# Kernel tuning notes

Hardware: AMD Instinct MI355X
Metric: run time of the kernel (lower is better)

## Reference

```python
import jax, jax.numpy as jnp
from jax import lax
import numpy as np

IN_SIZE, H_SIZE, OUT_SIZE, SEAS = 48, 128, 48, 24
DILATIONS = (1, 2, 4, 8)  # cells 0-1 = DRNN group 0, cells 2-3 = DRNN group 1


def setup_inputs() -> dict:
    key = jax.random.key(0)
    ks = jax.random.split(key, 16)
    B, T = 256, 512
    inp = {
        'train': jax.random.uniform(ks[0], (B, T), jnp.float32, 0.5, 1.5),
        'val': jax.random.uniform(ks[1], (B, OUT_SIZE), jnp.float32, 0.5, 1.5),
        'test': jax.random.uniform(ks[2], (B, OUT_SIZE), jnp.float32, 0.5, 1.5),
        'init_lev_sm': jnp.array([0.5], jnp.float32),
        'init_seas_sm': jnp.array([0.5], jnp.float32),
        'init_seasonalities': jnp.full((SEAS,), 0.5, jnp.float32),
    }
    cin = [IN_SIZE, H_SIZE, H_SIZE, H_SIZE]
    k = 3
    for i in range(4):
        inp[f'w_ih{i}'] = jax.random.normal(ks[k], (4 * H_SIZE, cin[i]), jnp.float32) * 0.05; k += 1
        inp[f'w_hh{i}'] = jax.random.normal(ks[k], (4 * H_SIZE, H_SIZE), jnp.float32) * 0.05; k += 1
        inp[f'b_ih{i}'] = jnp.zeros((4 * H_SIZE,), jnp.float32)
        inp[f'b_hh{i}'] = jnp.zeros((4 * H_SIZE,), jnp.float32)
    inp['nl_w'] = jax.random.normal(ks[k], (H_SIZE, H_SIZE), jnp.float32) * 0.05; k += 1
    inp['nl_b'] = jnp.zeros((H_SIZE,), jnp.float32)
    inp['sc_w'] = jax.random.normal(ks[k], (OUT_SIZE, H_SIZE), jnp.float32) * 0.05; k += 1
    inp['sc_b'] = jnp.zeros((OUT_SIZE,), jnp.float32)
    return inp


def _lstm(x, w_ih, w_hh, b_ih, b_hh):
    # x: (T, N, C) -> (T, N, H); torch LSTM gate order i, f, g, o
    n, h = x.shape[1], w_hh.shape[1]

    def step(carry, xt):
        hp, cp = carry
        g = xt @ w_ih.T + hp @ w_hh.T + (b_ih + b_hh)
        i, f, gg, o = jnp.split(g, 4, axis=-1)
        c = jax.nn.sigmoid(f) * cp + jax.nn.sigmoid(i) * jnp.tanh(gg)
        hn = jax.nn.sigmoid(o) * jnp.tanh(c)
        return (hn, c), hn

    z = jnp.zeros((n, h), x.dtype)
    _, hs = lax.scan(step, (z, z), x)
    return hs


def _dilated_lstm(x, d, w_ih, w_hh, b_ih, b_hh):
    # DRNN dilation: fold time by d into batch, run cell, unfold
    t, b, c = x.shape
    td = -(-t // d) * d
    xp = jnp.pad(x, ((0, td - t), (0, 0), (0, 0)))
    xd = xp.reshape(td // d, d, b, c).reshape(td // d, d * b, c)
    out = _lstm(xd, w_ih, w_hh, b_ih, b_hh)
    h = out.shape[-1]
    return out.reshape(td // d, d, b, h).reshape(td, b, h)[:t]


def _series_forward(data, cells, nl_w, nl_b, sc_w, sc_b):
    # ResidualDRNN: group 0 (cells 0,1), group 1 (cells 2,3) with residual add
    x = data
    for grp in range(2):
        res = x
        for ci in (2 * grp, 2 * grp + 1):
            x = _dilated_lstm(x, DILATIONS[ci], *cells[ci])
        if grp > 0:
            x = x + res
    x = jnp.tanh(x @ nl_w.T + nl_b)
    return x @ sc_w.T + sc_b


def _esrnn(train, val, init_lev_sm, init_seas_sm, init_seasonalities, cells, nl_w, nl_b, sc_w, sc_b):
    B, T = train.shape
    lev_sm = jax.nn.sigmoid(init_lev_sm[0])
    seas_sm = jax.nn.sigmoid(init_seas_sm[0])
    s0 = jnp.exp(init_seasonalities)  # (SEAS,) shared across series
    lev0 = train[:, 0] / s0[0]  # (B,)
    # rolling buffer: at step i it holds seasonalities[i .. i+SEAS-1]
    buf0 = jnp.broadcast_to(jnp.concatenate([s0[1:], s0[:1]])[:, None], (SEAS, B))

    def step(carry, x_t):
        lev_p, buf = carry
        seas_t = buf[0]
        lev_n = lev_sm * (x_t / seas_t) + (1 - lev_sm) * lev_p
        seas_n = seas_sm * (x_t / lev_n) + (1 - seas_sm) * seas_t
        return (lev_n, jnp.concatenate([buf[1:], seas_n[None]], 0)), (lev_n, seas_n)

    _, (levs_r, seas_r) = lax.scan(step, (lev0, buf0), train[:, 1:].T)
    levs = jnp.concatenate([lev0[None], levs_r], 0).T  # (B, T)
    seas_head = jnp.broadcast_to(jnp.concatenate([s0, s0[:1]])[:, None], (SEAS + 1, B))
    seas = jnp.concatenate([seas_head, seas_r], 0).T  # (B, T+SEAS)
    if OUT_SIZE > SEAS:  # seasonality extension branch
        start = seas.shape[1] - SEAS
        seas = jnp.concatenate([seas, seas[:, start:start + OUT_SIZE - SEAS]], 1)
    W = T - IN_SIZE + 1
    Wo = T - OUT_SIZE - IN_SIZE + 1
    idx_in = jnp.arange(W)[:, None] + jnp.arange(IN_SIZE)[None, :]  # (W, IN)
    win_in = (train[:, idx_in] / seas[:, idx_in] / levs[:, IN_SIZE - 1:, None]).transpose(1, 0, 2)  # (W,B,IN)
    idx_out = jnp.arange(Wo)[:, None] + IN_SIZE + jnp.arange(OUT_SIZE)[None, :]
    win_out = (train[:, idx_out] / seas[:, idx_out] / levs[:, IN_SIZE - 1:IN_SIZE - 1 + Wo, None]).transpose(1, 0, 2)
    network_pred = _series_forward(win_in[:-OUT_SIZE], cells, nl_w, nl_b, sc_w, sc_b)  # (Wo,B,OUT)
    network_act = win_out
    net_out_all = _series_forward(win_in, cells, nl_w, nl_b, sc_w, sc_b)  # (W,B,OUT)
    hold = net_out_all[-1] * seas[:, -OUT_SIZE:] * levs[:, -1:]
    hold_out_pred = hold * (hold > 0).astype(hold.dtype)
    hold_out_act = val  # testing=False path
    hold_out_act_norm = val / seas[:, -OUT_SIZE:] / levs[:, -1:]
    return network_pred, network_act, hold_out_pred, net_out_all, hold_out_act, hold_out_act_norm


def reference(train, val, test, init_lev_sm, init_seas_sm, init_seasonalities,
              w_ih0, w_hh0, b_ih0, b_hh0, w_ih1, w_hh1, b_ih1, b_hh1,
              w_ih2, w_hh2, b_ih2, b_hh2, w_ih3, w_hh3, b_ih3, b_hh3,
              nl_w, nl_b, sc_w, sc_b):
    cells = ((w_ih0, w_hh0, b_ih0, b_hh0), (w_ih1, w_hh1, b_ih1, b_hh1),
             (w_ih2, w_hh2, b_ih2, b_hh2), (w_ih3, w_hh3, b_ih3, b_hh3))
    return _esrnn(train, val, init_lev_sm, init_seas_sm, init_seasonalities,
                  cells, nl_w, nl_b, sc_w, sc_b)
```

## Files before the change

kernel.cpp:

```cpp
#include <hip/hip_runtime.h>
#include <cstdint>
#include <cstddef>

typedef _Float16 half8 __attribute__((ext_vector_type(8)));
typedef _Float16 half4 __attribute__((ext_vector_type(4)));
typedef float floatx4 __attribute__((ext_vector_type(4)));

namespace {
constexpr int kB = 256, kT = 512, kIN = 48, kOUT = 48, kSEAS = 24, kH = 128;
constexpr int kW = kT - kIN + 1;
constexpr int kWO = kT - kOUT - kIN + 1;
constexpr int kNB = kW * kB;
constexpr int kMBLK = kNB / 16;
constexpr float kLOG2E = 1.44269504088896340736f;
}

#if __has_builtin(__builtin_amdgcn_exp2f)
#define FEXP2(x) __builtin_amdgcn_exp2f(x)
#else
#define FEXP2(x) exp2f(x)
#endif
#if __has_builtin(__builtin_amdgcn_rcpf)
#define FRCP(x) __builtin_amdgcn_rcpf(x)
#else
#define FRCP(x) (1.0f / (x))
#endif

__device__ __forceinline__ float fsig(float y) { return FRCP(1.0f + FEXP2(-y)); }
__device__ __forceinline__ float ftanh(float x) { return 2.0f * fsig(2.0f * kLOG2E * x) - 1.0f; }

__global__ void k_transpose(const float* __restrict__ train, float* __restrict__ trainT) {
  int t = blockIdx.x, b = threadIdx.x;
  trainT[t * kB + b] = train[b * kT + t];
}

__global__ void k_es(const float* __restrict__ trainT, const float* __restrict__ levp,
                     const float* __restrict__ seasp, const float* __restrict__ inits,
                     float* __restrict__ seas, float* __restrict__ levs) {
  __shared__ float ring[kSEAS][kB];
  int b = threadIdx.x;
  float lev_sm = fsig(levp[0] * kLOG2E);
  float seas_sm = fsig(seasp[0] * kLOG2E);
  float s00 = expf(inits[0]);
  for (int s = 0; s < kSEAS; ++s) {
    float v = expf(inits[s]);
    seas[s * kB + b] = v;
    if (s >= 1) ring[s - 1][b] = v;
  }
  ring[kSEAS - 1][b] = s00;
  seas[kSEAS * kB + b] = s00;
  float lev = trainT[b] * FRCP(s00);
  levs[b] = lev;
  int rk = 0;
  float x_nx = trainT[kB + b];
  float st_nx = ring[0][b];
  for (int k = 0; k < kT - 1; ++k) {
    float x = x_nx;
    float st = st_nx;
    if (k + 1 < kT - 1) x_nx = trainT[(k + 2) * kB + b];
    int rn = (rk + 1 == kSEAS) ? 0 : rk + 1;
    st_nx = ring[rn][b];
    float ln = lev_sm * (x * FRCP(st)) + (1.0f - lev_sm) * lev;
    float sn = seas_sm * (x * FRCP(ln)) + (1.0f - seas_sm) * st;
    ring[rk][b] = sn;
    seas[(k + kSEAS + 1) * kB + b] = sn;
    levs[(k + 1) * kB + b] = ln;
    lev = ln;
    rk = rn;
  }
  for (int j = 0; j < kOUT - kSEAS; ++j)
    seas[(kT + kSEAS + j) * kB + b] = seas[(kT + j) * kB + b];
}

__global__ void k_win_in(const float* __restrict__ trainT, const float* __restrict__ seas,
                         const float* __restrict__ levs, _Float16* __restrict__ win) {
  int w = blockIdx.x;
  int tid = threadIdx.x;
#pragma unroll
  for (int i = 0; i < 16; ++i) {
    int o = i * 256 + tid;
    int b = o >> 3;
    int j0 = (o & 7) * 8;
    half8 h;
    if (j0 < kIN) {
      float rl = FRCP(levs[(kIN - 1 + w) * kB + b]);
#pragma unroll
      for (int jj = 0; jj < 8; ++jj) {
        int j = j0 + jj;
        int t = w + j;
        float v = (j < kIN) ? trainT[t * kB + b] * FRCP(seas[t * kB + b]) * rl : 0.0f;
        h[jj] = (_Float16)v;
      }
    } else {
#pragma unroll
      for (int jj = 0; jj < 8; ++jj) h[jj] = (_Float16)0.0f;
    }
    *(half8*)(win + ((size_t)(w * kB + b)) * 64 + j0) = h;
  }
}

__global__ void k_win_out(const float* __restrict__ trainT, const float* __restrict__ seas,
                          const float* __restrict__ levs, float* __restrict__ out1) {
  int idx = blockIdx.x * 256 + threadIdx.x;
  if (idx >= kWO * kB * (kOUT / 4)) return;
  int row = idx / 12;
  int j0 = (idx - row * 12) * 4;
  int wo = row >> 8;
  int b = row & 255;
  float rl = FRCP(levs[(kIN - 1 + wo) * kB + b]);
  floatx4 v;
#pragma unroll
  for (int jj = 0; jj < 4; ++jj) {
    int t = kIN + wo + j0 + jj;
    v[jj] = trainT[t * kB + b] * FRCP(seas[t * kB + b]) * rl;
  }
  *(floatx4*)(out1 + (size_t)row * kOUT + j0) = v;
}

__device__ __forceinline__ void prep_bias_elem(const float* bih, const float* bhh, float* dst,
                                               int c) {
  int ct = c >> 4, n16 = c & 15, g = ct & 3, wv = ct >> 2;
  int row = g * 128 + wv * 16 + n16;
  float sc = (g == 2) ? 2.0f * kLOG2E : kLOG2E;
  dst[c] = (bih[row] + bhh[row]) * sc;
}

__device__ __forceinline__ void prep_frag_elem(const float* Wsrc, _Float16* dst, int KB, int Kreal,
                                               int srcld, int perm, int idx) {
  int jj = idx & 7;
  int lane = (idx >> 3) & 63;
  int kb = (idx >> 9) % KB;
  int ct = idx / (KB * 512);
  int n16 = lane & 15;
  int k = kb * 32 + ((lane >> 4) << 3) + jj;
  int row;
  float sc;
  if (perm) {
    int g = ct & 3, wv = ct >> 2;
    row = g * 128 + wv * 16 + n16;
    sc = (g == 2) ? 2.0f * kLOG2E : kLOG2E;
  } else {
    row = ct * 16 + n16;
    sc = 1.0f;
  }
  float v = (k < Kreal) ? Wsrc[row * srcld + k] * sc : 0.0f;
  dst[idx] = (_Float16)v;
}

struct PrepArgs {
  const float* bih[4];
  const float* bhh[4];
  float* biasp[4];
  const float* wih[4];
  _Float16* wihf[4];
  const float* whh[4];
  _Float16* whhf[4];
  const float* nlw;
  _Float16* nlf;
  const float* scw;
  _Float16* scf;
};

__global__ void k_prep_all(PrepArgs a) {
  int seg = blockIdx.y;
  int idx = blockIdx.x * 256 + threadIdx.x;
  if (seg < 4) {
    if (idx < 512) prep_bias_elem(a.bih[seg], a.bhh[seg], a.biasp[seg], idx);
  } else if (seg == 4) {
    if (idx < 32 * 2 * 512) prep_frag_elem(a.wih[0], a.wihf[0], 2, 48, 48, 1, idx);
  } else if (seg < 8) {
    int c = seg - 4;
    if (idx < 32 * 4 * 512) prep_frag_elem(a.wih[c], a.wihf[c], 4, 128, 128, 1, idx);
  } else if (seg < 12) {
    int c = seg - 8;
    if (idx < 32 * 4 * 512) prep_frag_elem(a.whh[c], a.whhf[c], 4, 128, 128, 1, idx);
  } else if (seg == 12) {
    if (idx < 8 * 4 * 512) prep_frag_elem(a.nlw, a.nlf, 4, 128, 128, 0, idx);
  } else {
    if (idx < 3 * 4 * 512) prep_frag_elem(a.scw, a.scf, 4, 128, 128, 0, idx);
  }
}

__global__ void k_zero_prog(int* prog) {
  int i = threadIdx.x;
  if (i < 192) prog[i] = 0;
}

template <int NT, int KB, int MODE>
__global__ __launch_bounds__(512) void k_gemm(const _Float16* __restrict__ A,
                                              const _Float16* __restrict__ A2, int Khalfs,
                                              const _Float16* __restrict__ Bfr,
                                              const float* __restrict__ bias,
                                              _Float16* __restrict__ outh,
                                              float* __restrict__ outf,
                                              float* __restrict__ outf2) {
  __shared__ _Float16 bsh[NT * KB * 512];
  int tid = threadIdx.x;
  {
    const uint4* src = (const uint4*)Bfr;
    uint4* dst = (uint4*)bsh;
    for (int i = tid; i < NT * KB * 64; i += 512) dst[i] = src[i];
  }
  __syncthreads();
  int wv = tid >> 6, lane = tid & 63;
  int mblk = blockIdx.x * 8 + wv;
  if (mblk >= kMBLK) return;
  int m = lane & 15, kq = lane >> 4;
  const _Float16* arow = A + (size_t)(mblk * 16 + m) * Khalfs + kq * 8;
  half8 af[KB];
#pragma unroll
  for (int kb = 0; kb < KB; ++kb) af[kb] = *(const half8*)(arow + kb * 32);
  if constexpr (MODE == 1) {
    const _Float16* arow2 = A2 + (size_t)(mblk * 16 + m) * Khalfs + kq * 8;
#pragma unroll
    for (int kb = 0; kb < KB; ++kb) {
      half8 a2 = *(const half8*)(arow2 + kb * 32);
      af[kb] += a2;
    }
  }
#pragma unroll
  for (int t0 = 0; t0 < NT; t0 += 2) {
    float b0 = bias[t0 * 16 + m];
    floatx4 acc0 = {b0, b0, b0, b0};
    floatx4 acc1 = {0.f, 0.f, 0.f, 0.f};
    if (t0 + 1 < NT) {
      float b1 = bias[(t0 + 1) * 16 + m];
      acc1 = (floatx4){b1, b1, b1, b1};
    }
#pragma unroll
    for (int kb = 0; kb < KB; ++kb) {
      half8 bf0 = *(const half8*)(&bsh[((t0 * KB + kb) * 64 + lane) * 8]);
      acc0 = __builtin_amdgcn_mfma_f32_16x16x32_f16(af[kb], bf0, acc0, 0, 0, 0);
      if (t0 + 1 < NT) {
        half8 bf1 = *(const half8*)(&bsh[(((t0 + 1) * KB + kb) * 64 + lane) * 8]);
        acc1 = __builtin_amdgcn_mfma_f32_16x16x32_f16(af[kb], bf1, acc1, 0, 0, 0);
      }
    }
    if constexpr (MODE == 1) {
#pragma unroll
      for (int r = 0; r < 4; ++r) {
        int row = mblk * 16 + kq * 4 + r;
        outh[(size_t)row * kH + t0 * 16 + m] = (_Float16)ftanh(acc0[r]);
        if (t0 + 1 < NT) outh[(size_t)row * kH + (t0 + 1) * 16 + m] = (_Float16)ftanh(acc1[r]);
      }
    } else {
#pragma unroll
      for (int r = 0; r < 4; ++r) {
        int row = mblk * 16 + kq * 4 + r;
        float v0 = acc0[r];
        outf[(size_t)row * kOUT + t0 * 16 + m] = v0;
        if (row < kWO * kB) outf2[(size_t)row * kOUT + t0 * 16 + m] = v0;
        if (t0 + 1 < NT) {
          float v1 = acc1[r];
          outf[(size_t)row * kOUT + (t0 + 1) * 16 + m] = v1;
          if (row < kWO * kB) outf2[(size_t)row * kOUT + (t0 + 1) * 16 + m] = v1;
        }
      }
    }
  }
}

struct FArgs {
  const _Float16* win;
  const _Float16* wihf[4];
  const _Float16* whhf[4];
  const float* biasp[4];
  _Float16* H[4];
  int* prog;
};

__device__ __forceinline__ void wait_prog(int* p, int need, int& fenced, int* obs_sh) {
  if (need <= fenced) return;
  if (threadIdx.x == 0) {
    int v;
    while ((v = __hip_atomic_load(p, __ATOMIC_RELAXED, __HIP_MEMORY_SCOPE_AGENT)) < need)
      __builtin_amdgcn_s_sleep(16);
    *obs_sh = v;
  }
  __syncthreads();
  int v = *obs_sh;
  __builtin_amdgcn_fence(__ATOMIC_ACQUIRE, "agent");
  fenced = v;
}

template <int KXB, bool POLL, bool REL>
__device__ __forceinline__ void floop(const _Float16* __restrict__ Xsrc,
                                      const _Float16* __restrict__ wihp,
                                      const _Float16* __restrict__ whhp,
                                      const float* __restrict__ bp, _Float16* __restrict__ Hout,
                                      int* progIn, int sprev, int* progOut, int d, int kd, int ib,
                                      _Float16 (*hbuf)[2048], int* obs_sh) {
  int tid = threadIdx.x;
  int wv = tid >> 6, lane = tid & 63, m = lane & 15, kq = lane >> 4;
  half8 wxf[4][KXB], whf[4][4];
#pragma unroll
  for (int g = 0; g < 4; ++g) {
#pragma unroll
    for (int kb = 0; kb < KXB; ++kb)
      wxf[g][kb] = *(const half8*)(wihp + ((((wv * 4 + g) * KXB + kb) * 64 + lane) * 8));
#pragma unroll
    for (int kb = 0; kb < 4; ++kb)
      whf[g][kb] = *(const half8*)(whhp + ((((wv * 4 + g) * 4 + kb) * 64 + lane) * 8));
  }
  float bg[4];
#pragma unroll
  for (int g = 0; g < 4; ++g) bg[g] = bp[(wv * 4 + g) * 16 + m];
  float cc[4] = {0.f, 0.f, 0.f, 0.f};
  int nsteps = (kW - kd + d - 1) / d;
  const int xstride = KXB * 32;
  int fenced = 0;
  if (POLL) wait_prog(progIn + (kd & ((1 << sprev) - 1)), (kd >> sprev) + 1, fenced, obs_sh);
  half8 hxc[KXB], hxn[KXB];
  {
    const _Float16* xr = Xsrc + (size_t)(kd * kB + ib * 16 + m) * xstride + kq * 8;
#pragma unroll
    for (int kb = 0; kb < KXB; ++kb) hxc[kb] = *(const half8*)(xr + kb * 32);
  }
  for (int j = 0; j < nsteps; ++j) {
    int ph = j & 1;
    int wtn = (j + 1) * d + kd;
    bool havenext = (j + 1 < nsteps);
    if (POLL && havenext)
      wait_prog(progIn + (wtn & ((1 << sprev) - 1)), (wtn >> sprev) + 1, fenced, obs_sh);
    floatx4 acc[4];
#pragma unroll
    for (int g = 0; g < 4; ++g) acc[g] = (floatx4){bg[g], bg[g], bg[g], bg[g]};
    if (havenext) {
      const _Float16* xr = Xsrc + (size_t)(wtn * kB + ib * 16 + m) * xstride + kq * 8;
#pragma unroll
      for (int kb = 0; kb < KXB; ++kb) hxn[kb] = *(const half8*)(xr + kb * 32);
    }
#pragma unroll
    for (int kb = 0; kb < KXB; ++kb)
#pragma unroll
      for (int g = 0; g < 4; ++g)
        acc[g] = __builtin_amdgcn_mfma_f32_16x16x32_f16(hxc[kb], wxf[g][kb], acc[g], 0, 0, 0);
    if (j > 0) {
#pragma unroll
      for (int kb = 0; kb < 4; ++kb) {
        int gran = (kb * 4 + kq) ^ m;
        half8 a = *(const half8*)(&hbuf[ph ^ 1][m * 128 + gran * 8]);
#pragma unroll
        for (int g = 0; g < 4; ++g)
          acc[g] = __builtin_amdgcn_mfma_f32_16x16x32_f16(a, whf[g][kb], acc[g], 0, 0, 0);
      }
    }
#pragma unroll
    for (int r = 0; r < 4; ++r) {
      float iv = fsig(acc[0][r]);
      float fv = fsig(acc[1][r]);
      float g2 = fsig(acc[2][r]);
      float ov = fsig(acc[3][r]);
      cc[r] = fv * cc[r] + iv * (2.0f * g2 - 1.0f);
      float tc = 2.0f * fsig(cc[r] * (2.0f * kLOG2E)) - 1.0f;
      float hv = ov * tc;
      int brow = kq * 4 + r;
      int hu = wv * 16 + m;
      int gran = (hu >> 3) ^ brow;
      hbuf[ph][brow * 128 + gran * 8 + (hu & 7)] = (_Float16)hv;
    }
    __syncthreads();
    {
      int hr = tid >> 5, hu0 = (tid & 31) * 4;
      int gran = (hu0 >> 3) ^ hr;
      half4 hv4 = *(const half4*)(&hbuf[ph][hr * 128 + gran * 8 + (hu0 & 7)]);
      *(half4*)(Hout + (size_t)((j * d + kd) * kB + ib * 16 + hr) * kH + hu0) = hv4;
    }
    if (REL && (((j & 7) == 7) || (j + 1 == nsteps))) {
      __syncthreads();
      if (tid == 0)
        __hip_atomic_store(progOut, j + 1, __ATOMIC_RELEASE, __HIP_MEMORY_SCOPE_AGENT);
    }
#pragma unroll
    for (int kb = 0; kb < KXB; ++kb) hxc[kb] = hxn[kb];
  }
}

__global__ __launch_bounds__(512) void k_fused(FArgs a) {
  __shared__ _Float16 hbuf[2][2048];
  __shared__ int obs_sh;
  int w = blockIdx.x;
  int cell, d, kd, ib;
  if (w < 16) {
    cell = 0; d = 1; kd = 0; ib = w;
  } else if (w < 48) {
    cell = 1; d = 2; kd = (w - 16) >> 4; ib = (w - 16) & 15;
  } else if (w < 112) {
    cell = 2; d = 4; kd = (w - 48) >> 4; ib = (w - 48) & 15;
  } else {
    cell = 3; d = 8; kd = (w - 112) >> 4; ib = (w - 112) & 15;
  }
  const _Float16* Xsrc = (cell == 0) ? a.win : a.H[cell - 1];
  _Float16* Hout = a.H[cell];
  int* progOut = a.prog + (cell * 16 + ib) * 4 + kd;
  int* progIn = (cell > 0) ? a.prog + ((cell - 1) * 16 + ib) * 4 : nullptr;
  int sprev = (cell == 2) ? 1 : ((cell == 3) ? 2 : 0);
  if (cell == 0)
    floop<2, false, true>(Xsrc, a.wihf[0], a.whhf[0], a.biasp[0], Hout, nullptr, 0, progOut, d,
                          kd, ib, hbuf, &obs_sh);
  else if (cell < 3)
    floop<4, true, true>(Xsrc, a.wihf[cell], a.whhf[cell], a.biasp[cell], Hout, progIn, sprev,
                         progOut, d, kd, ib, hbuf, &obs_sh);
  else
    floop<4, true, false>(Xsrc, a.wihf[3], a.whhf[3], a.biasp[3], Hout, progIn, sprev, progOut,
                          d, kd, ib, hbuf, &obs_sh);
}

__global__ void k_tail(const float* __restrict__ out3, const float* __restrict__ val,
                       const float* __restrict__ seas, const float* __restrict__ levs,
                       float* __restrict__ out2, float* __restrict__ out4,
                       float* __restrict__ out5) {
  int idx = blockIdx.x * 256 + threadIdx.x;
  int b = idx / kOUT, j = idx % kOUT;
  float s = seas[(kT + j) * kB + b];
  float L = levs[(kT - 1) * kB + b];
  float net = out3[(size_t)(kW - 1) * kB * kOUT + idx];
  float hp = net * s * L;
  out2[idx] = hp > 0.0f ? hp : 0.0f;
  float v = val[idx];
  out4[idx] = v;
  out5[idx] = v / s / L;
}

extern "C" void kernel_launch(void* const* d_in, const int* in_sizes, int n_in, void* d_out,
                              int out_size, void* d_ws, size_t ws_size, hipStream_t stream) {
  const float* train = (const float*)d_in[0];
  const float* val = (const float*)d_in[1];
  const float* levp = (const float*)d_in[3];
  const float* seasp = (const float*)d_in[4];
  const float* inits = (const float*)d_in[5];
  const float* w_ih[4] = {(const float*)d_in[6], (const float*)d_in[10], (const float*)d_in[14],
                          (const float*)d_in[18]};
  const float* w_hh[4] = {(const float*)d_in[7], (const float*)d_in[11], (const float*)d_in[15],
                          (const float*)d_in[19]};
  const float* b_ih[4] = {(const float*)d_in[8], (const float*)d_in[12], (const float*)d_in[16],
                          (const float*)d_in[20]};
  const float* b_hh[4] = {(const float*)d_in[9], (const float*)d_in[13], (const float*)d_in[17],
                          (const float*)d_in[21]};
  const float* nl_w = (const float*)d_in[22];
  const float* nl_b = (const float*)d_in[23];
  const float* sc_w = (const float*)d_in[24];
  const float* sc_b = (const float*)d_in[25];

  char* wsb = (char*)d_ws;
  size_t off = 0;
  auto alloc = [&](size_t bytes) -> void* {
    void* p = wsb + off;
    off = (off + bytes + 255) & ~(size_t)255;
    return p;
  };
  float* trainT = (float*)alloc((size_t)kT * kB * 4);
  float* seas = (float*)alloc((size_t)560 * kB * 4);
  float* levs = (float*)alloc((size_t)kT * kB * 4);
  _Float16* win = (_Float16*)alloc((size_t)kNB * 64 * 2);
  _Float16* Hc[4];
  for (int c = 0; c < 4; ++c) Hc[c] = (_Float16*)alloc((size_t)kNB * kH * 2);
  _Float16* U = (_Float16*)alloc((size_t)kNB * kH * 2);
  float* biasp[4];
  for (int c = 0; c < 4; ++c) biasp[c] = (float*)alloc(512 * 4);
  _Float16* wihf[4];
  wihf[0] = (_Float16*)alloc((size_t)32 * 2 * 512 * 2);
  for (int c = 1; c < 4; ++c) wihf[c] = (_Float16*)alloc((size_t)32 * 4 * 512 * 2);
  _Float16* whhf[4];
  for (int c = 0; c < 4; ++c) whhf[c] = (_Float16*)alloc((size_t)32 * 4 * 512 * 2);
  _Float16* nlf = (_Float16*)alloc((size_t)8 * 4 * 512 * 2);
  _Float16* scf = (_Float16*)alloc((size_t)3 * 4 * 512 * 2);
  int* prog = (int*)alloc(192 * 4);

  float* out0 = (float*)d_out;
  float* out1 = out0 + (size_t)kWO * kB * kOUT;
  float* out2 = out1 + (size_t)kWO * kB * kOUT;
  float* out3 = out2 + (size_t)kB * kOUT;
  float* out4 = out3 + (size_t)kW * kB * kOUT;
  float* out5 = out4 + (size_t)kB * kOUT;

  k_transpose<<<kT, kB, 0, stream>>>(train, trainT);
  k_es<<<1, kB, 0, stream>>>(trainT, levp, seasp, inits, seas, levs);
  k_win_in<<<kW, kB, 0, stream>>>(trainT, seas, levs, win);
  k_win_out<<<(kWO * kB * 12 + 255) / 256, 256, 0, stream>>>(trainT, seas, levs, out1);

  PrepArgs pa;
  for (int c = 0; c < 4; ++c) {
    pa.bih[c] = b_ih[c]; pa.bhh[c] = b_hh[c]; pa.biasp[c] = biasp[c];
    pa.wih[c] = w_ih[c]; pa.wihf[c] = wihf[c];
    pa.whh[c] = w_hh[c]; pa.whhf[c] = whhf[c];
  }
  pa.nlw = nl_w; pa.nlf = nlf; pa.scw = sc_w; pa.scf = scf;
  k_prep_all<<<dim3(256, 14), 256, 0, stream>>>(pa);
  k_zero_prog<<<1, 256, 0, stream>>>(prog);

  FArgs fa;
  fa.win = win;
  for (int c = 0; c < 4; ++c) {
    fa.wihf[c] = wihf[c]; fa.whhf[c] = whhf[c]; fa.biasp[c] = biasp[c]; fa.H[c] = Hc[c];
  }
  fa.prog = prog;
  void* kp[1] = {(void*)&fa};
  hipLaunchCooperativeKernel((void*)k_fused, dim3(240), dim3(512), kp, 0, stream);

  const int GG = kMBLK / 8;
  k_gemm<8, 4, 1><<<GG, 512, 0, stream>>>(Hc[3], Hc[1], 128, nlf, nl_b, U, nullptr, nullptr);
  k_gemm<3, 4, 2><<<GG, 512, 0, stream>>>(U, nullptr, 128, scf, sc_b, nullptr, out3, out0);
  k_tail<<<48, 256, 0, stream>>>(out3, val, seas, levs, out2, out4, out5);
}
```

Measured before the change: 712.3 us.

## Precompute cell-0 input projection with a batched GEMM before recurrent loop

Adds a GEMM pass that computes the input-to-gate projection plus bias for the first LSTM cell over all timesteps, stored in MFMA fragment layout as fp16. The recurrent cell-0 loop then loads these precomputed gate values instead of running the input MFMAs on its critical path. H stores also change from a shared-memory staged half4 write to direct per-lane scalar writes. The cost is an extra kernel launch and buffer traffic, and the preactivations are now rounded to fp16.

Measured after the change: 758.5 us. +6.5%, slower.

```diff
diff --git a/kernel.cpp b/kernel.cpp
--- a/kernel.cpp
+++ b/kernel.cpp
@@ -236,7 +236,14 @@
         acc1 = __builtin_amdgcn_mfma_f32_16x16x32_f16(af[kb], bf1, acc1, 0, 0, 0);
       }
     }
-    if constexpr (MODE == 1) {
+    if constexpr (MODE == 0) {
+      half4 h0 = {(_Float16)acc0[0], (_Float16)acc0[1], (_Float16)acc0[2], (_Float16)acc0[3]};
+      *(half4*)(outh + (((size_t)mblk * NT + t0) * 64 + lane) * 4) = h0;
+      if (t0 + 1 < NT) {
+        half4 h1 = {(_Float16)acc1[0], (_Float16)acc1[1], (_Float16)acc1[2], (_Float16)acc1[3]};
+        *(half4*)(outh + (((size_t)mblk * NT + (t0 + 1)) * 64 + lane) * 4) = h1;
+      }
+    } else if constexpr (MODE == 1) {
 #pragma unroll
       for (int r = 0; r < 4; ++r) {
         int row = mblk * 16 + kq * 4 + r;
@@ -261,6 +268,7 @@
 }
 
 struct FArgs {
+  const _Float16* xfr;
   const _Float16* win;
   const _Float16* wihf[4];
   const _Float16* whhf[4];
@@ -283,7 +291,7 @@
   fenced = v;
 }
 
-template <int KXB, bool POLL, bool REL>
+template <int KXB, bool POLL, bool REL, bool XPRE>
 __device__ __forceinline__ void floop(const _Float16* __restrict__ Xsrc,
                                       const _Float16* __restrict__ wihp,
                                       const _Float16* __restrict__ whhp,
@@ -295,26 +303,36 @@
   half8 wxf[4][KXB], whf[4][4];
 #pragma unroll
   for (int g = 0; g < 4; ++g) {
-#pragma unroll
-    for (int kb = 0; kb < KXB; ++kb)
-      wxf[g][kb] = *(const half8*)(wihp + ((((wv * 4 + g) * KXB + kb) * 64 + lane) * 8));
+    if (!XPRE) {
+#pragma unroll
+      for (int kb = 0; kb < KXB; ++kb)
+        wxf[g][kb] = *(const half8*)(wihp + ((((wv * 4 + g) * KXB + kb) * 64 + lane) * 8));
+    }
 #pragma unroll
     for (int kb = 0; kb < 4; ++kb)
       whf[g][kb] = *(const half8*)(whhp + ((((wv * 4 + g) * 4 + kb) * 64 + lane) * 8));
   }
   float bg[4];
-#pragma unroll
-  for (int g = 0; g < 4; ++g) bg[g] = bp[(wv * 4 + g) * 16 + m];
+  if (!XPRE) {
+#pragma unroll
+    for (int g = 0; g < 4; ++g) bg[g] = bp[(wv * 4 + g) * 16 + m];
+  }
   float cc[4] = {0.f, 0.f, 0.f, 0.f};
   int nsteps = (kW - kd + d - 1) / d;
   const int xstride = KXB * 32;
   int fenced = 0;
   if (POLL) wait_prog(progIn + (kd & ((1 << sprev) - 1)), (kd >> sprev) + 1, fenced, obs_sh);
   half8 hxc[KXB], hxn[KXB];
-  {
-    const _Float16* xr = Xsrc + (size_t)(kd * kB + ib * 16 + m) * xstride + kq * 8;
-#pragma unroll
-    for (int kb = 0; kb < KXB; ++kb) hxc[kb] = *(const half8*)(xr + kb * 32);
+  half4 xr[4], xrn[4];
+  if (XPRE) {
+    int mb = kd * 16 + ib;
+#pragma unroll
+    for (int g = 0; g < 4; ++g)
+      xr[g] = *(const half4*)(Xsrc + (((size_t)mb * 32 + (wv * 4 + g)) * 64 + lane) * 4);
+  } else {
+    const _Float16* xrow = Xsrc + (size_t)(kd * kB + ib * 16 + m) * xstride + kq * 8;
+#pragma unroll
+    for (int kb = 0; kb < KXB; ++kb) hxc[kb] = *(const half8*)(xrow + kb * 32);
   }
   for (int j = 0; j < nsteps; ++j) {
     int ph = j & 1;
@@ -323,18 +341,33 @@
     if (POLL && havenext)
       wait_prog(progIn + (wtn & ((1 << sprev) - 1)), (wtn >> sprev) + 1, fenced, obs_sh);
     floatx4 acc[4];
-#pragma unroll
-    for (int g = 0; g < 4; ++g) acc[g] = (floatx4){bg[g], bg[g], bg[g], bg[g]};
+    if (XPRE) {
+#pragma unroll
+      for (int g = 0; g < 4; ++g)
+        acc[g] = (floatx4){(float)xr[g][0], (float)xr[g][1], (float)xr[g][2], (float)xr[g][3]};
+    } else {
+#pragma unroll
+      for (int g = 0; g < 4; ++g) acc[g] = (floatx4){bg[g], bg[g], bg[g], bg[g]};
+    }
     if (havenext) {
-      const _Float16* xr = Xsrc + (size_t)(wtn * kB + ib * 16 + m) * xstride + kq * 8;
-#pragma unroll
-      for (int kb = 0; kb < KXB; ++kb) hxn[kb] = *(const half8*)(xr + kb * 32);
-    }
-#pragma unroll
-    for (int kb = 0; kb < KXB; ++kb)
-#pragma unroll
-      for (int g = 0; g < 4; ++g)
-        acc[g] = __builtin_amdgcn_mfma_f32_16x16x32_f16(hxc[kb], wxf[g][kb], acc[g], 0, 0, 0);
+      if (XPRE) {
+        int mb = wtn * 16 + ib;
+#pragma unroll
+        for (int g = 0; g < 4; ++g)
+          xrn[g] = *(const half4*)(Xsrc + (((size_t)mb * 32 + (wv * 4 + g)) * 64 + lane) * 4);
+      } else {
+        const _Float16* xrow = Xsrc + (size_t)(wtn * kB + ib * 16 + m) * xstride + kq * 8;
+#pragma unroll
+        for (int kb = 0; kb < KXB; ++kb) hxn[kb] = *(const half8*)(xrow + kb * 32);
+      }
+    }
+    if (!XPRE) {
+#pragma unroll
+      for (int kb = 0; kb < KXB; ++kb)
+#pragma unroll
+        for (int g = 0; g < 4; ++g)
+          acc[g] = __builtin_amdgcn_mfma_f32_16x16x32_f16(hxc[kb], wxf[g][kb], acc[g], 0, 0, 0);
+    }
     if (j > 0) {
 #pragma unroll
       for (int kb = 0; kb < 4; ++kb) {
@@ -345,6 +378,7 @@
           acc[g] = __builtin_amdgcn_mfma_f32_16x16x32_f16(a, whf[g][kb], acc[g], 0, 0, 0);
       }
     }
+    _Float16 hv[4];
 #pragma unroll
     for (int r = 0; r < 4; ++r) {
       float iv = fsig(acc[0][r]);
@@ -353,26 +387,31 @@
       float ov = fsig(acc[3][r]);
       cc[r] = fv * cc[r] + iv * (2.0f * g2 - 1.0f);
       float tc = 2.0f * fsig(cc[r] * (2.0f * kLOG2E)) - 1.0f;
-      float hv = ov * tc;
+      hv[r] = (_Float16)(ov * tc);
       int brow = kq * 4 + r;
       int hu = wv * 16 + m;
       int gran = (hu >> 3) ^ brow;
-      hbuf[ph][brow * 128 + gran * 8 + (hu & 7)] = (_Float16)hv;
+      hbuf[ph][brow * 128 + gran * 8 + (hu & 7)] = hv[r];
     }
     __syncthreads();
     {
-      int hr = tid >> 5, hu0 = (tid & 31) * 4;
-      int gran = (hu0 >> 3) ^ hr;
-      half4 hv4 = *(const half4*)(&hbuf[ph][hr * 128 + gran * 8 + (hu0 & 7)]);
-      *(half4*)(Hout + (size_t)((j * d + kd) * kB + ib * 16 + hr) * kH + hu0) = hv4;
+      int hu = wv * 16 + m;
+      size_t rb = (size_t)((j * d + kd) * kB + ib * 16 + kq * 4);
+#pragma unroll
+      for (int r = 0; r < 4; ++r) Hout[(rb + r) * kH + hu] = hv[r];
     }
     if (REL && (((j & 7) == 7) || (j + 1 == nsteps))) {
       __syncthreads();
       if (tid == 0)
         __hip_atomic_store(progOut, j + 1, __ATOMIC_RELEASE, __HIP_MEMORY_SCOPE_AGENT);
     }
-#pragma unroll
-    for (int kb = 0; kb < KXB; ++kb) hxc[kb] = hxn[kb];
+    if (XPRE) {
+#pragma unroll
+      for (int g = 0; g < 4; ++g) xr[g] = xrn[g];
+    } else {
+#pragma unroll
+      for (int kb = 0; kb < KXB; ++kb) hxc[kb] = hxn[kb];
+    }
   }
 }
 
@@ -390,20 +429,19 @@
   } else {
     cell = 3; d = 8; kd = (w - 112) >> 4; ib = (w - 112) & 15;
   }
-  const _Float16* Xsrc = (cell == 0) ? a.win : a.H[cell - 1];
   _Float16* Hout = a.H[cell];
   int* progOut = a.prog + (cell * 16 + ib) * 4 + kd;
   int* progIn = (cell > 0) ? a.prog + ((cell - 1) * 16 + ib) * 4 : nullptr;
   int sprev = (cell == 2) ? 1 : ((cell == 3) ? 2 : 0);
   if (cell == 0)
-    floop<2, false, true>(Xsrc, a.wihf[0], a.whhf[0], a.biasp[0], Hout, nullptr, 0, progOut, d,
-                          kd, ib, hbuf, &obs_sh);
+    floop<2, false, true, true>(a.xfr, nullptr, a.whhf[0], nullptr, Hout, nullptr, 0, progOut,
+                                d, kd, ib, hbuf, &obs_sh);
   else if (cell < 3)
-    floop<4, true, true>(Xsrc, a.wihf[cell], a.whhf[cell], a.biasp[cell], Hout, progIn, sprev,
-                         progOut, d, kd, ib, hbuf, &obs_sh);
+    floop<4, true, true, false>(a.H[cell - 1], a.wihf[cell], a.whhf[cell], a.biasp[cell], Hout,
+                                progIn, sprev, progOut, d, kd, ib, hbuf, &obs_sh);
   else
-    floop<4, true, false>(Xsrc, a.wihf[3], a.whhf[3], a.biasp[3], Hout, progIn, sprev, progOut,
-                          d, kd, ib, hbuf, &obs_sh);
+    floop<4, true, false, false>(a.H[2], a.wihf[3], a.whhf[3], a.biasp[3], Hout, progIn, sprev,
+                                 progOut, d, kd, ib, hbuf, &obs_sh);
 }
 
 __global__ void k_tail(const float* __restrict__ out3, const float* __restrict__ val,
@@ -453,9 +491,9 @@
   float* seas = (float*)alloc((size_t)560 * kB * 4);
   float* levs = (float*)alloc((size_t)kT * kB * 4);
   _Float16* win = (_Float16*)alloc((size_t)kNB * 64 * 2);
+  _Float16* Xfr = (_Float16*)alloc((size_t)kMBLK * 32 * 64 * 4 * 2);
   _Float16* Hc[4];
   for (int c = 0; c < 4; ++c) Hc[c] = (_Float16*)alloc((size_t)kNB * kH * 2);
-  _Float16* U = (_Float16*)alloc((size_t)kNB * kH * 2);
   float* biasp[4];
   for (int c = 0; c < 4; ++c) biasp[c] = (float*)alloc(512 * 4);
   _Float16* wihf[4];
@@ -466,6 +504,7 @@
   _Float16* nlf = (_Float16*)alloc((size_t)8 * 4 * 512 * 2);
   _Float16* scf = (_Float16*)alloc((size_t)3 * 4 * 512 * 2);
   int* prog = (int*)alloc(192 * 4);
+  _Float16* U = Xfr;
 
   float* out0 = (float*)d_out;
   float* out1 = out0 + (size_t)kWO * kB * kOUT;
@@ -489,7 +528,12 @@
   k_prep_all<<<dim3(256, 14), 256, 0, stream>>>(pa);
   k_zero_prog<<<1, 256, 0, stream>>>(prog);
 
+  const int GG = kMBLK / 8;
+  k_gemm<32, 2, 0><<<GG, 512, 0, stream>>>(win, nullptr, 64, wihf[0], biasp[0], Xfr, nullptr,
+                                           nullptr);
+
   FArgs fa;
+  fa.xfr = Xfr;
   fa.win = win;
   for (int c = 0; c < 4; ++c) {
     fa.wihf[c] = wihf[c]; fa.whhf[c] = whhf[c]; fa.biasp[c] = biasp[c]; fa.H[c] = Hc[c];
@@ -498,7 +542,6 @@
   void* kp[1] = {(void*)&fa};
   hipLaunchCooperativeKernel((void*)k_fused, dim3(240), dim3(512), kp, 0, stream);
 
-  const int GG = kMBLK / 8;
   k_gemm<8, 4, 1><<<GG, 512, 0, stream>>>(Hc[3], Hc[1], 128, nlf, nl_b, U, nullptr, nullptr);
   k_gemm<3, 4, 2><<<GG, 512, 0, stream>>>(U, nullptr, 128, scf, sc_b, nullptr, out3, out0);
   k_tail<<<48, 256, 0, stream>>>(out3, val, seas, levs, out2, out4, out5);
```

## Process two batch tiles per workgroup in fused dilated LSTM kernel

Applied to the files above, without the earlier changes.

Halves the cooperative grid so each workgroup runs two independent 16-row batch tiles, interleaving their MFMA chains to hide the per-step recurrence latency. Gate math is reworked to share reciprocals across sigmoid/tanh products. The LDS round-trip for H output is replaced by direct global stores, and the barrier uses an explicit lgkmcnt wait. The x prefetch is dropped for the polling cells, so their input loads now sit on the critical path after each wait, and the halved grid uses fewer CUs.

Result: slower. 1.058 ms (+48.5%).

```diff
diff --git a/kernel.cpp b/kernel.cpp
--- a/kernel.cpp
+++ b/kernel.cpp
@@ -25,6 +25,8 @@
 #else
 #define FRCP(x) (1.0f / (x))
 #endif
+
+#define LGKM_BARRIER() asm volatile("s_waitcnt lgkmcnt(0)\n\ts_barrier" ::: "memory")
 
 __device__ __forceinline__ float fsig(float y) { return FRCP(1.0f + FEXP2(-y)); }
 __device__ __forceinline__ float ftanh(float x) { return 2.0f * fsig(2.0f * kLOG2E * x) - 1.0f; }
@@ -182,8 +184,7 @@
 }
 
 __global__ void k_zero_prog(int* prog) {
-  int i = threadIdx.x;
-  if (i < 192) prog[i] = 0;
+  prog[threadIdx.x] = 0;
 }
 
 template <int NT, int KB, int MODE>
@@ -269,13 +270,15 @@
   int* prog;
 };
 
-__device__ __forceinline__ void wait_prog(int* p, int need, int& fenced, int* obs_sh) {
+__device__ __forceinline__ void wait2(int* pA, int* pB, int need, int& fenced, int* obs_sh) {
   if (need <= fenced) return;
   if (threadIdx.x == 0) {
-    int v;
-    while ((v = __hip_atomic_load(p, __ATOMIC_RELAXED, __HIP_MEMORY_SCOPE_AGENT)) < need)
+    int vA, vB;
+    while ((vA = __hip_atomic_load(pA, __ATOMIC_RELAXED, __HIP_MEMORY_SCOPE_AGENT)) < need)
       __builtin_amdgcn_s_sleep(16);
-    *obs_sh = v;
+    while ((vB = __hip_atomic_load(pB, __ATOMIC_RELAXED, __HIP_MEMORY_SCOPE_AGENT)) < need)
+      __builtin_amdgcn_s_sleep(16);
+    *obs_sh = vA < vB ? vA : vB;
   }
   __syncthreads();
   int v = *obs_sh;
@@ -283,13 +286,15 @@
   fenced = v;
 }
 
-template <int KXB, bool POLL, bool REL>
-__device__ __forceinline__ void floop(const _Float16* __restrict__ Xsrc,
-                                      const _Float16* __restrict__ wihp,
-                                      const _Float16* __restrict__ whhp,
-                                      const float* __restrict__ bp, _Float16* __restrict__ Hout,
-                                      int* progIn, int sprev, int* progOut, int d, int kd, int ib,
-                                      _Float16 (*hbuf)[2048], int* obs_sh) {
+template <int KXB, bool POLL, bool REL, bool XPF>
+__device__ __forceinline__ void floop2(const _Float16* __restrict__ Xsrc,
+                                       const _Float16* __restrict__ wihp,
+                                       const _Float16* __restrict__ whhp,
+                                       const float* __restrict__ bp,
+                                       _Float16* __restrict__ Hout, int* progInA, int* progInB,
+                                       int sprev, int* progOutA, int* progOutB, int d, int kd,
+                                       int ibA, int ibB, _Float16 (*hbuf)[2][2048],
+                                       int* obs_sh) {
   int tid = threadIdx.x;
   int wv = tid >> 6, lane = tid & 63, m = lane & 15, kq = lane >> 4;
   half8 wxf[4][KXB], whf[4][4];
@@ -305,105 +310,178 @@
   float bg[4];
 #pragma unroll
   for (int g = 0; g < 4; ++g) bg[g] = bp[(wv * 4 + g) * 16 + m];
-  float cc[4] = {0.f, 0.f, 0.f, 0.f};
+  float ccA[4] = {0.f, 0.f, 0.f, 0.f}, ccB[4] = {0.f, 0.f, 0.f, 0.f};
   int nsteps = (kW - kd + d - 1) / d;
   const int xstride = KXB * 32;
   int fenced = 0;
-  if (POLL) wait_prog(progIn + (kd & ((1 << sprev) - 1)), (kd >> sprev) + 1, fenced, obs_sh);
-  half8 hxc[KXB], hxn[KXB];
-  {
-    const _Float16* xr = Xsrc + (size_t)(kd * kB + ib * 16 + m) * xstride + kq * 8;
-#pragma unroll
-    for (int kb = 0; kb < KXB; ++kb) hxc[kb] = *(const half8*)(xr + kb * 32);
+  half8 hxcA[KXB], hxcB[KXB], hxnA[KXB], hxnB[KXB];
+  if (XPF) {
+    const _Float16* xrA = Xsrc + (size_t)(kd * kB + ibA * 16 + m) * xstride + kq * 8;
+    const _Float16* xrB = Xsrc + (size_t)(kd * kB + ibB * 16 + m) * xstride + kq * 8;
+#pragma unroll
+    for (int kb = 0; kb < KXB; ++kb) {
+      hxcA[kb] = *(const half8*)(xrA + kb * 32);
+      hxcB[kb] = *(const half8*)(xrB + kb * 32);
+    }
   }
   for (int j = 0; j < nsteps; ++j) {
     int ph = j & 1;
-    int wtn = (j + 1) * d + kd;
-    bool havenext = (j + 1 < nsteps);
-    if (POLL && havenext)
-      wait_prog(progIn + (wtn & ((1 << sprev) - 1)), (wtn >> sprev) + 1, fenced, obs_sh);
-    floatx4 acc[4];
-#pragma unroll
-    for (int g = 0; g < 4; ++g) acc[g] = (floatx4){bg[g], bg[g], bg[g], bg[g]};
-    if (havenext) {
-      const _Float16* xr = Xsrc + (size_t)(wtn * kB + ib * 16 + m) * xstride + kq * 8;
-#pragma unroll
-      for (int kb = 0; kb < KXB; ++kb) hxn[kb] = *(const half8*)(xr + kb * 32);
-    }
-#pragma unroll
-    for (int kb = 0; kb < KXB; ++kb)
-#pragma unroll
-      for (int g = 0; g < 4; ++g)
-        acc[g] = __builtin_amdgcn_mfma_f32_16x16x32_f16(hxc[kb], wxf[g][kb], acc[g], 0, 0, 0);
+    int wt = j * d + kd;
+    if (POLL) {
+      int kdp = wt & ((1 << sprev) - 1), need = (wt >> sprev) + 1;
+      wait2(progInA + kdp, progInB + kdp, need, fenced, obs_sh);
+    }
+    if (!XPF) {
+      const _Float16* xrA = Xsrc + (size_t)(wt * kB + ibA * 16 + m) * xstride + kq * 8;
+      const _Float16* xrB = Xsrc + (size_t)(wt * kB + ibB * 16 + m) * xstride + kq * 8;
+#pragma unroll
+      for (int kb = 0; kb < KXB; ++kb) {
+        hxcA[kb] = *(const half8*)(xrA + kb * 32);
+        hxcB[kb] = *(const half8*)(xrB + kb * 32);
+      }
+    } else if (j + 1 < nsteps) {
+      int wtn = wt + d;
+      const _Float16* xrA = Xsrc + (size_t)(wtn * kB + ibA * 16 + m) * xstride + kq * 8;
+      const _Float16* xrB = Xsrc + (size_t)(wtn * kB + ibB * 16 + m) * xstride + kq * 8;
+#pragma unroll
+      for (int kb = 0; kb < KXB; ++kb) {
+        hxnA[kb] = *(const half8*)(xrA + kb * 32);
+        hxnB[kb] = *(const half8*)(xrB + kb * 32);
+      }
+    }
+    half8 aA[4], aB[4];
     if (j > 0) {
 #pragma unroll
       for (int kb = 0; kb < 4; ++kb) {
         int gran = (kb * 4 + kq) ^ m;
-        half8 a = *(const half8*)(&hbuf[ph ^ 1][m * 128 + gran * 8]);
+        aA[kb] = *(const half8*)(&hbuf[0][ph ^ 1][m * 128 + gran * 8]);
+        aB[kb] = *(const half8*)(&hbuf[1][ph ^ 1][m * 128 + gran * 8]);
+      }
+    }
+    floatx4 accA[4], accB[4];
+#pragma unroll
+    for (int g = 0; g < 4; ++g) {
+      accA[g] = (floatx4){bg[g], bg[g], bg[g], bg[g]};
+      accB[g] = (floatx4){bg[g], bg[g], bg[g], bg[g]};
+    }
+#pragma unroll
+    for (int kb = 0; kb < KXB; ++kb)
+#pragma unroll
+      for (int g = 0; g < 4; ++g)
+        accA[g] = __builtin_amdgcn_mfma_f32_16x16x32_f16(hxcA[kb], wxf[g][kb], accA[g], 0, 0, 0);
+    if (j > 0) {
+#pragma unroll
+      for (int kb = 0; kb < 4; ++kb)
 #pragma unroll
         for (int g = 0; g < 4; ++g)
-          acc[g] = __builtin_amdgcn_mfma_f32_16x16x32_f16(a, whf[g][kb], acc[g], 0, 0, 0);
-      }
-    }
+          accA[g] = __builtin_amdgcn_mfma_f32_16x16x32_f16(aA[kb], whf[g][kb], accA[g], 0, 0, 0);
+    }
+#pragma unroll
+    for (int kb = 0; kb < KXB; ++kb)
+#pragma unroll
+      for (int g = 0; g < 4; ++g)
+        accB[g] = __builtin_amdgcn_mfma_f32_16x16x32_f16(hxcB[kb], wxf[g][kb], accB[g], 0, 0, 0);
+    if (j > 0) {
+#pragma unroll
+      for (int kb = 0; kb < 4; ++kb)
+#pragma unroll
+        for (int g = 0; g < 4; ++g)
+          accB[g] = __builtin_amdgcn_mfma_f32_16x16x32_f16(aB[kb], whf[g][kb], accB[g], 0, 0, 0);
+    }
+    _Float16 hvA[4], hvB[4];
 #pragma unroll
     for (int r = 0; r < 4; ++r) {
-      float iv = fsig(acc[0][r]);
-      float fv = fsig(acc[1][r]);
-      float g2 = fsig(acc[2][r]);
-      float ov = fsig(acc[3][r]);
-      cc[r] = fv * cc[r] + iv * (2.0f * g2 - 1.0f);
-      float tc = 2.0f * fsig(cc[r] * (2.0f * kLOG2E)) - 1.0f;
-      float hv = ov * tc;
+      float ea = FEXP2(-accA[0][r]);
+      float ef = FEXP2(-accA[1][r]);
+      float eb = FEXP2(-accA[2][r]);
+      float eo = FEXP2(-accA[3][r]);
+      float fv = FRCP(1.0f + ef);
+      float it = (1.0f - eb) * FRCP((1.0f + ea) * (1.0f + eb));
+      ccA[r] = fv * ccA[r] + it;
+      float ed = FEXP2(ccA[r] * (-2.0f * kLOG2E));
+      hvA[r] = (_Float16)((1.0f - ed) * FRCP((1.0f + eo) * (1.0f + ed)));
+    }
+#pragma unroll
+    for (int r = 0; r < 4; ++r) {
+      float ea = FEXP2(-accB[0][r]);
+      float ef = FEXP2(-accB[1][r]);
+      float eb = FEXP2(-accB[2][r]);
+      float eo = FEXP2(-accB[3][r]);
+      float fv = FRCP(1.0f + ef);
+      float it = (1.0f - eb) * FRCP((1.0f + ea) * (1.0f + eb));
+      ccB[r] = fv * ccB[r] + it;
+      float ed = FEXP2(ccB[r] * (-2.0f * kLOG2E));
+      hvB[r] = (_Float16)((1.0f - ed) * FRCP((1.0f + eo) * (1.0f + ed)));
+    }
+#pragma unroll
+    for (int r = 0; r < 4; ++r) {
       int brow = kq * 4 + r;
       int hu = wv * 16 + m;
       int gran = (hu >> 3) ^ brow;
-      hbuf[ph][brow * 128 + gran * 8 + (hu & 7)] = (_Float16)hv;
-    }
-    __syncthreads();
+      hbuf[0][ph][brow * 128 + gran * 8 + (hu & 7)] = hvA[r];
+      hbuf[1][ph][brow * 128 + gran * 8 + (hu & 7)] = hvB[r];
+    }
+    LGKM_BARRIER();
     {
-      int hr = tid >> 5, hu0 = (tid & 31) * 4;
-      int gran = (hu0 >> 3) ^ hr;
-      half4 hv4 = *(const half4*)(&hbuf[ph][hr * 128 + gran * 8 + (hu0 & 7)]);
-      *(half4*)(Hout + (size_t)((j * d + kd) * kB + ib * 16 + hr) * kH + hu0) = hv4;
+      int hu = wv * 16 + m;
+      size_t rbA = (size_t)(wt * kB + ibA * 16 + kq * 4);
+      size_t rbB = (size_t)(wt * kB + ibB * 16 + kq * 4);
+#pragma unroll
+      for (int r = 0; r < 4; ++r) {
+        Hout[(rbA + r) * kH + hu] = hvA[r];
+        Hout[(rbB + r) * kH + hu] = hvB[r];
+      }
     }
     if (REL && (((j & 7) == 7) || (j + 1 == nsteps))) {
       __syncthreads();
-      if (tid == 0)
-        __hip_atomic_store(progOut, j + 1, __ATOMIC_RELEASE, __HIP_MEMORY_SCOPE_AGENT);
-    }
-#pragma unroll
-    for (int kb = 0; kb < KXB; ++kb) hxc[kb] = hxn[kb];
+      if (tid == 0) {
+        __hip_atomic_store(progOutA, j + 1, __ATOMIC_RELEASE, __HIP_MEMORY_SCOPE_AGENT);
+        __hip_atomic_store(progOutB, j + 1, __ATOMIC_RELEASE, __HIP_MEMORY_SCOPE_AGENT);
+      }
+    }
+    if (XPF) {
+#pragma unroll
+      for (int kb = 0; kb < KXB; ++kb) {
+        hxcA[kb] = hxnA[kb];
+        hxcB[kb] = hxnB[kb];
+      }
+    }
   }
 }
 
 __global__ __launch_bounds__(512) void k_fused(FArgs a) {
-  __shared__ _Float16 hbuf[2][2048];
+  __shared__ _Float16 hbuf[2][2][2048];
   __shared__ int obs_sh;
   int w = blockIdx.x;
-  int cell, d, kd, ib;
-  if (w < 16) {
-    cell = 0; d = 1; kd = 0; ib = w;
-  } else if (w < 48) {
-    cell = 1; d = 2; kd = (w - 16) >> 4; ib = (w - 16) & 15;
-  } else if (w < 112) {
-    cell = 2; d = 4; kd = (w - 48) >> 4; ib = (w - 48) & 15;
+  int cell, d, kd, ip;
+  if (w < 8) {
+    cell = 0; d = 1; kd = 0; ip = w;
+  } else if (w < 24) {
+    cell = 1; d = 2; int idx = w - 8; kd = idx >> 3; ip = idx & 7;
+  } else if (w < 56) {
+    cell = 2; d = 4; int idx = w - 24; kd = idx >> 3; ip = idx & 7;
   } else {
-    cell = 3; d = 8; kd = (w - 112) >> 4; ib = (w - 112) & 15;
-  }
+    cell = 3; d = 8; int idx = w - 56; kd = idx >> 3; ip = idx & 7;
+  }
+  int ibA = ip * 2, ibB = ip * 2 + 1;
   const _Float16* Xsrc = (cell == 0) ? a.win : a.H[cell - 1];
   _Float16* Hout = a.H[cell];
-  int* progOut = a.prog + (cell * 16 + ib) * 4 + kd;
-  int* progIn = (cell > 0) ? a.prog + ((cell - 1) * 16 + ib) * 4 : nullptr;
+  int* progOutA = a.prog + (cell * 16 + ibA) * 4 + kd;
+  int* progOutB = a.prog + (cell * 16 + ibB) * 4 + kd;
+  int* progInA = (cell > 0) ? a.prog + ((cell - 1) * 16 + ibA) * 4 : nullptr;
+  int* progInB = (cell > 0) ? a.prog + ((cell - 1) * 16 + ibB) * 4 : nullptr;
   int sprev = (cell == 2) ? 1 : ((cell == 3) ? 2 : 0);
   if (cell == 0)
-    floop<2, false, true>(Xsrc, a.wihf[0], a.whhf[0], a.biasp[0], Hout, nullptr, 0, progOut, d,
-                          kd, ib, hbuf, &obs_sh);
+    floop2<2, false, true, true>(Xsrc, a.wihf[0], a.whhf[0], a.biasp[0], Hout, nullptr, nullptr,
+                                 0, progOutA, progOutB, d, kd, ibA, ibB, hbuf, &obs_sh);
   else if (cell < 3)
-    floop<4, true, true>(Xsrc, a.wihf[cell], a.whhf[cell], a.biasp[cell], Hout, progIn, sprev,
-                         progOut, d, kd, ib, hbuf, &obs_sh);
+    floop2<4, true, true, false>(Xsrc, a.wihf[cell], a.whhf[cell], a.biasp[cell], Hout, progInA,
+                                 progInB, sprev, progOutA, progOutB, d, kd, ibA, ibB, hbuf,
+                                 &obs_sh);
   else
-    floop<4, true, false>(Xsrc, a.wihf[3], a.whhf[3], a.biasp[3], Hout, progIn, sprev, progOut,
-                          d, kd, ib, hbuf, &obs_sh);
+    floop2<4, true, false, false>(Xsrc, a.wihf[3], a.whhf[3], a.biasp[3], Hout, progInA,
+                                  progInB, sprev, progOutA, progOutB, d, kd, ibA, ibB, hbuf,
+                                  &obs_sh);
 }
 
 __global__ void k_tail(const float* __restrict__ out3, const float* __restrict__ val,
@@ -465,7 +543,7 @@
   for (int c = 0; c < 4; ++c) whhf[c] = (_Float16*)alloc((size_t)32 * 4 * 512 * 2);
   _Float16* nlf = (_Float16*)alloc((size_t)8 * 4 * 512 * 2);
   _Float16* scf = (_Float16*)alloc((size_t)3 * 4 * 512 * 2);
-  int* prog = (int*)alloc(192 * 4);
+  int* prog = (int*)alloc(256 * 4);
 
   float* out0 = (float*)d_out;
   float* out1 = out0 + (size_t)kWO * kB * kOUT;
@@ -496,7 +574,7 @@
   }
   fa.prog = prog;
   void* kp[1] = {(void*)&fa};
-  hipLaunchCooperativeKernel((void*)k_fused, dim3(240), dim3(512), kp, 0, stream);
+  hipLaunchCooperativeKernel((void*)k_fused, dim3(120), dim3(512), kp, 0, stream);
 
   const int GG = kMBLK / 8;
   k_gemm<8, 4, 1><<<GG, 512, 0, stream>>>(Hc[3], Hc[1], 128, nlf, nl_b, U, nullptr, nullptr);
```

## Precompute next-step input projection off the recurrent critical path in fused LSTM

Applied to the files above, without the earlier changes.

The input-to-hidden MFMA products for the next timestep are now computed after the current step's hidden state is produced, so the serial recurrence only does the hidden-to-hidden MFMAs before the gate math. Gate activations are reworked to share reciprocals (fewer rcp calls), and the H output is written directly from registers instead of a second LDS read after a full __syncthreads. The barrier is replaced by an inline s_waitcnt lgkmcnt(0) + s_barrier that does not wait on global stores. The Hout stores are now scattered 2-byte writes instead of coalesced half4 writes. The lighter barrier's memory-ordering behaviour relative to the release store is a risk.

New measurement: 737.9 us. +3.6%, slower.

```diff
diff --git a/kernel.cpp b/kernel.cpp
--- a/kernel.cpp
+++ b/kernel.cpp
@@ -25,6 +25,8 @@
 #else
 #define FRCP(x) (1.0f / (x))
 #endif
+
+#define LGKM_BARRIER() asm volatile("s_waitcnt lgkmcnt(0)\n\ts_barrier" ::: "memory")
 
 __device__ __forceinline__ float fsig(float y) { return FRCP(1.0f + FEXP2(-y)); }
 __device__ __forceinline__ float ftanh(float x) { return 2.0f * fsig(2.0f * kLOG2E * x) - 1.0f; }
@@ -182,8 +184,7 @@
 }
 
 __global__ void k_zero_prog(int* prog) {
-  int i = threadIdx.x;
-  if (i < 192) prog[i] = 0;
+  prog[threadIdx.x] = 0;
 }
 
 template <int NT, int KB, int MODE>
@@ -310,69 +311,90 @@
   const int xstride = KXB * 32;
   int fenced = 0;
   if (POLL) wait_prog(progIn + (kd & ((1 << sprev) - 1)), (kd >> sprev) + 1, fenced, obs_sh);
-  half8 hxc[KXB], hxn[KXB];
+  floatx4 xacc[4];
   {
-    const _Float16* xr = Xsrc + (size_t)(kd * kB + ib * 16 + m) * xstride + kq * 8;
-#pragma unroll
-    for (int kb = 0; kb < KXB; ++kb) hxc[kb] = *(const half8*)(xr + kb * 32);
+    const _Float16* xrow = Xsrc + (size_t)(kd * kB + ib * 16 + m) * xstride + kq * 8;
+    half8 hx[KXB];
+#pragma unroll
+    for (int kb = 0; kb < KXB; ++kb) hx[kb] = *(const half8*)(xrow + kb * 32);
+#pragma unroll
+    for (int g = 0; g < 4; ++g) {
+      xacc[g] = (floatx4){bg[g], bg[g], bg[g], bg[g]};
+#pragma unroll
+      for (int kb = 0; kb < KXB; ++kb)
+        xacc[g] = __builtin_amdgcn_mfma_f32_16x16x32_f16(hx[kb], wxf[g][kb], xacc[g], 0, 0, 0);
+    }
   }
   for (int j = 0; j < nsteps; ++j) {
     int ph = j & 1;
-    int wtn = (j + 1) * d + kd;
+    int wt = j * d + kd;
+    int wtn = wt + d;
     bool havenext = (j + 1 < nsteps);
     if (POLL && havenext)
       wait_prog(progIn + (wtn & ((1 << sprev) - 1)), (wtn >> sprev) + 1, fenced, obs_sh);
+    half8 hx[KXB];
+    if (havenext) {
+      const _Float16* xrow = Xsrc + (size_t)(wtn * kB + ib * 16 + m) * xstride + kq * 8;
+#pragma unroll
+      for (int kb = 0; kb < KXB; ++kb) hx[kb] = *(const half8*)(xrow + kb * 32);
+    }
     floatx4 acc[4];
-#pragma unroll
-    for (int g = 0; g < 4; ++g) acc[g] = (floatx4){bg[g], bg[g], bg[g], bg[g]};
-    if (havenext) {
-      const _Float16* xr = Xsrc + (size_t)(wtn * kB + ib * 16 + m) * xstride + kq * 8;
-#pragma unroll
-      for (int kb = 0; kb < KXB; ++kb) hxn[kb] = *(const half8*)(xr + kb * 32);
-    }
-#pragma unroll
-    for (int kb = 0; kb < KXB; ++kb)
-#pragma unroll
-      for (int g = 0; g < 4; ++g)
-        acc[g] = __builtin_amdgcn_mfma_f32_16x16x32_f16(hxc[kb], wxf[g][kb], acc[g], 0, 0, 0);
     if (j > 0) {
+      half8 a[4];
 #pragma unroll
       for (int kb = 0; kb < 4; ++kb) {
         int gran = (kb * 4 + kq) ^ m;
-        half8 a = *(const half8*)(&hbuf[ph ^ 1][m * 128 + gran * 8]);
+        a[kb] = *(const half8*)(&hbuf[ph ^ 1][m * 128 + gran * 8]);
+      }
+#pragma unroll
+      for (int g = 0; g < 4; ++g) acc[g] = xacc[g];
+#pragma unroll
+      for (int kb = 0; kb < 4; ++kb)
 #pragma unroll
         for (int g = 0; g < 4; ++g)
-          acc[g] = __builtin_amdgcn_mfma_f32_16x16x32_f16(a, whf[g][kb], acc[g], 0, 0, 0);
-      }
-    }
+          acc[g] = __builtin_amdgcn_mfma_f32_16x16x32_f16(a[kb], whf[g][kb], acc[g], 0, 0, 0);
+    } else {
+#pragma unroll
+      for (int g = 0; g < 4; ++g) acc[g] = xacc[g];
+    }
+    _Float16 hv[4];
 #pragma unroll
     for (int r = 0; r < 4; ++r) {
-      float iv = fsig(acc[0][r]);
-      float fv = fsig(acc[1][r]);
-      float g2 = fsig(acc[2][r]);
-      float ov = fsig(acc[3][r]);
-      cc[r] = fv * cc[r] + iv * (2.0f * g2 - 1.0f);
-      float tc = 2.0f * fsig(cc[r] * (2.0f * kLOG2E)) - 1.0f;
-      float hv = ov * tc;
+      float ea = FEXP2(-acc[0][r]);
+      float ef = FEXP2(-acc[1][r]);
+      float eb = FEXP2(-acc[2][r]);
+      float eo = FEXP2(-acc[3][r]);
+      float fv = FRCP(1.0f + ef);
+      float it = (1.0f - eb) * FRCP((1.0f + ea) * (1.0f + eb));
+      cc[r] = fv * cc[r] + it;
+      float ed = FEXP2(cc[r] * (-2.0f * kLOG2E));
+      hv[r] = (_Float16)((1.0f - ed) * FRCP((1.0f + eo) * (1.0f + ed)));
       int brow = kq * 4 + r;
       int hu = wv * 16 + m;
       int gran = (hu >> 3) ^ brow;
-      hbuf[ph][brow * 128 + gran * 8 + (hu & 7)] = (_Float16)hv;
-    }
-    __syncthreads();
+      hbuf[ph][brow * 128 + gran * 8 + (hu & 7)] = hv[r];
+    }
     {
-      int hr = tid >> 5, hu0 = (tid & 31) * 4;
-      int gran = (hu0 >> 3) ^ hr;
-      half4 hv4 = *(const half4*)(&hbuf[ph][hr * 128 + gran * 8 + (hu0 & 7)]);
-      *(half4*)(Hout + (size_t)((j * d + kd) * kB + ib * 16 + hr) * kH + hu0) = hv4;
-    }
+      int hu = wv * 16 + m;
+      size_t rb = (size_t)(wt * kB + ib * 16 + kq * 4);
+#pragma unroll
+      for (int r = 0; r < 4; ++r) Hout[(rb + r) * kH + hu] = hv[r];
+    }
+    if (havenext) {
+#pragma unroll
+      for (int g = 0; g < 4; ++g) {
+        xacc[g] = (floatx4){bg[g], bg[g], bg[g], bg[g]};
+#pragma unroll
+        for (int kb = 0; kb < KXB; ++kb)
+          xacc[g] = __builtin_amdgcn_mfma_f32_16x16x32_f16(hx[kb], wxf[g][kb], xacc[g], 0, 0, 0);
+      }
+    }
+    LGKM_BARRIER();
     if (REL && (((j & 7) == 7) || (j + 1 == nsteps))) {
       __syncthreads();
       if (tid == 0)
         __hip_atomic_store(progOut, j + 1, __ATOMIC_RELEASE, __HIP_MEMORY_SCOPE_AGENT);
     }
-#pragma unroll
-    for (int kb = 0; kb < KXB; ++kb) hxc[kb] = hxn[kb];
   }
 }
 
@@ -465,7 +487,7 @@
   for (int c = 0; c < 4; ++c) whhf[c] = (_Float16*)alloc((size_t)32 * 4 * 512 * 2);
   _Float16* nlf = (_Float16*)alloc((size_t)8 * 4 * 512 * 2);
   _Float16* scf = (_Float16*)alloc((size_t)3 * 4 * 512 * 2);
-  int* prog = (int*)alloc(192 * 4);
+  int* prog = (int*)alloc(256 * 4);
 
   float* out0 = (float*)d_out;
   float* out1 = out0 + (size_t)kWO * kB * kOUT;
```
